# Performance work log

Measured on AMD Instinct MI355X. Metric: run time of the kernel, lower is better.

The kernel has to match this reference:

```python
import jax, jax.numpy as jnp
import numpy as np

N_NODES = 100000
N_EDGES = 1600000
MSG = 16
HID = 16
N_ETYPE = 8
N_CLASSES = 40


def setup_inputs() -> dict:
    key = jax.random.key(0)
    ks = jax.random.split(key, 11)
    return {
        "features": jax.random.normal(ks[0], (N_NODES, HID), dtype=jnp.float32),
        "src": jax.random.randint(ks[1], (N_EDGES,), 0, N_NODES),
        "dst": jax.random.randint(ks[2], (N_EDGES,), 0, N_NODES),
        "etype": jax.random.randint(ks[3], (N_EDGES,), 0, N_ETYPE),
        "edge_matrix": jax.random.normal(ks[4], (N_ETYPE, MSG * HID), dtype=jnp.float32) * 0.1,
        "w_ih": jax.random.normal(ks[5], (3 * HID, MSG), dtype=jnp.float32) * 0.1,
        "w_hh": jax.random.normal(ks[6], (3 * HID, HID), dtype=jnp.float32) * 0.1,
        "b_ih": jax.random.normal(ks[7], (3 * HID,), dtype=jnp.float32) * 0.1,
        "b_hh": jax.random.normal(ks[8], (3 * HID,), dtype=jnp.float32) * 0.1,
        "out_w": jax.random.normal(ks[9], (N_CLASSES, HID), dtype=jnp.float32) * 0.1,
        "out_b": jax.random.normal(ks[10], (N_CLASSES,), dtype=jnp.float32) * 0.1,
    }


def reference(features, src, dst, etype, edge_matrix, w_ih, w_hh, b_ih, b_hh, out_w, out_b):
    n = features.shape[0]
    # message: per-edge [MSG,HID] matrix (gathered by edge type) times src h
    A = edge_matrix[etype].reshape(-1, MSG, HID)          # [E, MSG, HID]
    msg = jnp.einsum('emh,eh->em', A, features[src])      # [E, MSG]
    # reduce: scatter-sum messages onto destination nodes
    m = jax.ops.segment_sum(msg, dst, num_segments=n)     # [N, MSG]
    # apply: one GRU step per node (PyTorch nn.GRU gate math)
    gi = m @ w_ih.T + b_ih                                # [N, 3*HID]
    gh = features @ w_hh.T + b_hh                         # [N, 3*HID]
    i_r, i_z, i_n = jnp.split(gi, 3, axis=-1)
    h_r, h_z, h_n = jnp.split(gh, 3, axis=-1)
    r = jax.nn.sigmoid(i_r + h_r)
    z = jax.nn.sigmoid(i_z + h_z)
    c = jnp.tanh(i_n + r * h_n)
    h = (1.0 - z) * c + z * features                      # [N, HID]
    return h @ out_w.T + out_b                            # [N, N_CLASSES]
```

## Files before the change

### kernel.cpp

```cpp
#include <hip/hip_runtime.h>
#include <math.h>

constexpr int N_NODES   = 100000;
constexpr int N_EDGES   = 1600000;
constexpr int MSG       = 16;
constexpr int HID       = 16;
constexpr int N_ETYPE   = 8;
constexpr int N_CLASSES = 40;

constexpr int CBSIZE   = 256;
constexpr int NBUCKET  = (N_NODES + CBSIZE - 1) / CBSIZE;
constexpr int SBSIZE   = 32;
constexpr int NSUB     = 8;
constexpr int NSB      = NBUCKET * NSUB;
constexpr int EPB      = 4096;
constexpr int NEBLK    = (N_EDGES + EPB - 1) / EPB;
constexpr int REC_CAP  = 5120;
constexpr int FGRID    = 1536;
constexpr int NSLOT    = 2048;
constexpr int A_STRIDE = 260;
constexpr int SRECC    = 1536;

typedef float vfloat4 __attribute__((ext_vector_type(4)));

__device__ __forceinline__ float sigmoidf_(float x) { return 1.0f / (1.0f + __expf(-x)); }
__device__ __forceinline__ float tanhf_(float x) { float e = __expf(2.0f * x); return 1.0f - 2.0f / (e + 1.0f); }

__device__ __forceinline__ unsigned f2bf(float f) {
    unsigned u = __float_as_uint(f);
    return (u + 0x7FFFu + ((u >> 16) & 1u)) >> 16;
}
__device__ __forceinline__ float bflo(unsigned u) { return __uint_as_float(u << 16); }
__device__ __forceinline__ float bfhi(unsigned u) { return __uint_as_float(u & 0xFFFF0000u); }

__global__ void __launch_bounds__(256) cvt_kernel(const float* __restrict__ features,
                                                  uint4* __restrict__ featb,
                                                  int* __restrict__ gcursor) {
    int i = blockIdx.x * 256 + threadIdx.x;
    if (i < NBUCKET) gcursor[i] = i * REC_CAP;
    else if (i == NBUCKET) gcursor[i] = FGRID;
    if (i * 8 >= N_NODES * HID) return;
    const float4* fp = reinterpret_cast<const float4*>(features + i * 8);
    float4 a = fp[0], b = fp[1];
    uint4 o;
    o.x = f2bf(a.x) | (f2bf(a.y) << 16);
    o.y = f2bf(a.z) | (f2bf(a.w) << 16);
    o.z = f2bf(b.x) | (f2bf(b.y) << 16);
    o.w = f2bf(b.z) | (f2bf(b.w) << 16);
    featb[i] = o;
}

__global__ void __launch_bounds__(512) partition_kernel(
    const int* __restrict__ src,
    const int* __restrict__ dst,
    const int* __restrict__ etype,
    int* __restrict__ gcursor,
    int* __restrict__ records)
{
    __shared__ int srec[EPB];
    __shared__ unsigned short sbkt[EPB];
    __shared__ int lh[NBUCKET];
    __shared__ int lscan[NBUCKET];
    __shared__ int gbarr[NBUCKET];
    __shared__ int wsum[8];

    int t = threadIdx.x;
    int base = blockIdx.x * EPB;

    for (int i = t; i < NBUCKET; i += 512) lh[i] = 0;
    __syncthreads();

    int rr[8]; int bb[8]; int rk[8];
    #pragma unroll
    for (int q = 0; q < 8; ++q) {
        int e = base + t + 512 * q;
        if (e < N_EDGES) {
            int d = dst[e];
            bb[q] = d >> 8;
            rr[q] = (src[e] << 11) | (etype[e] << 8) | (d & 255);
            rk[q] = atomicAdd(&lh[bb[q]], 1);
        } else bb[q] = -1;
    }
    __syncthreads();

    int i0 = t * 4;
    int v0 = 0, v1 = 0, v2 = 0, v3 = 0;
    if (i0     < NBUCKET) v0 = lh[i0];
    if (i0 + 1 < NBUCKET) v1 = lh[i0 + 1];
    if (i0 + 2 < NBUCKET) v2 = lh[i0 + 2];
    if (i0 + 3 < NBUCKET) v3 = lh[i0 + 3];
    int tsum = v0 + v1 + v2 + v3;

    int lane = t & 63, w = t >> 6;
    int inc = tsum;
    #pragma unroll
    for (int off = 1; off < 64; off <<= 1) {
        int u = __shfl_up(inc, off, 64);
        if (lane >= off) inc += u;
    }
    if (lane == 63) wsum[w] = inc;
    __syncthreads();
    int basew = 0;
    #pragma unroll
    for (int i = 0; i < 8; ++i) if (i < w) basew += wsum[i];
    int excl = basew + inc - tsum;

    if (i0     < NBUCKET) { lscan[i0]     = excl; gbarr[i0]     = v0 ? atomicAdd(&gcursor[i0],     v0) : 0; } excl += v0;
    if (i0 + 1 < NBUCKET) { lscan[i0 + 1] = excl; gbarr[i0 + 1] = v1 ? atomicAdd(&gcursor[i0 + 1], v1) : 0; } excl += v1;
    if (i0 + 2 < NBUCKET) { lscan[i0 + 2] = excl; gbarr[i0 + 2] = v2 ? atomicAdd(&gcursor[i0 + 2], v2) : 0; } excl += v2;
    if (i0 + 3 < NBUCKET) { lscan[i0 + 3] = excl; gbarr[i0 + 3] = v3 ? atomicAdd(&gcursor[i0 + 3], v3) : 0; }
    __syncthreads();

    #pragma unroll
    for (int q = 0; q < 8; ++q) {
        if (bb[q] >= 0) {
            int sidx = lscan[bb[q]] + rk[q];
            srec[sidx] = rr[q];
            sbkt[sidx] = (unsigned short)bb[q];
        }
    }
    __syncthreads();

    int cnt = min(EPB, N_EDGES - base);
    for (int s2 = t; s2 < cnt; s2 += 512) {
        int b2 = sbkt[s2];
        int pos = gbarr[b2] + (s2 - lscan[b2]);
        if (pos < (b2 + 1) * REC_CAP)
            records[pos] = srec[s2];
    }
}

__global__ void __launch_bounds__(256) partition2_kernel(
    const int* __restrict__ gcursor,
    const int* __restrict__ records,
    int* __restrict__ records2,
    int* __restrict__ slot_off)
{
    __shared__ int hist[NSLOT];
    __shared__ int wsum[4];
    __shared__ int srec[REC_CAP];

    int cb = blockIdx.x;
    int beg = cb * REC_CAP;
    int cnt = min(gcursor[cb] - beg, REC_CAP);
    int t = threadIdx.x;

    #pragma unroll
    for (int j = 0; j < 8; ++j) hist[t * 8 + j] = 0;
    __syncthreads();

    for (int i = t; i < cnt; i += 256) {
        int r = records[beg + i];
        atomicAdd(&hist[((r & 255) << 3) | ((r >> 8) & 7)], 1);
    }
    __syncthreads();

    int loc[8]; int tsum = 0;
    #pragma unroll
    for (int j = 0; j < 8; ++j) { loc[j] = hist[t * 8 + j]; tsum += loc[j]; }

    int lane = t & 63, w = t >> 6;
    int inc = tsum;
    #pragma unroll
    for (int off = 1; off < 64; off <<= 1) {
        int u = __shfl_up(inc, off, 64);
        if (lane >= off) inc += u;
    }
    if (lane == 63) wsum[w] = inc;
    __syncthreads();
    int basew = 0;
    #pragma unroll
    for (int i = 0; i < 4; ++i) if (i < w) basew += wsum[i];
    int excl = basew + inc - tsum;

    #pragma unroll
    for (int j = 0; j < 8; ++j) {
        slot_off[cb * (NSLOT + 1) + t * 8 + j] = beg + excl;
        hist[t * 8 + j] = excl;
        excl += loc[j];
    }
    if (t == 0) slot_off[cb * (NSLOT + 1) + NSLOT] = beg + cnt;
    __syncthreads();

    for (int i = t; i < cnt; i += 256) {
        int r = records[beg + i];
        int pos = atomicAdd(&hist[((r & 255) << 3) | ((r >> 8) & 7)], 1);
        srec[pos] = r;
    }
    __syncthreads();
    for (int i = t; i < cnt; i += 256) records2[beg + i] = srec[i];
}

__global__ void __launch_bounds__(256, 6) fused_kernel(
    const uint4* __restrict__ featb,
    const float* __restrict__ features,
    const int*   __restrict__ slot_off,
    const int*   __restrict__ records2,
    int*         __restrict__ wcnt,
    const float* __restrict__ edge_matrix,
    const float* __restrict__ w_ih,
    const float* __restrict__ w_hh,
    const float* __restrict__ b_ih,
    const float* __restrict__ b_hh,
    const float* __restrict__ out_w,
    const float* __restrict__ out_b,
    float*       __restrict__ out)
{
    __shared__ float A[N_ETYPE * A_STRIDE];
    __shared__ float wihL[3 * HID * 17];
    __shared__ float whhL[3 * HID * 17];
    __shared__ float outwL[N_CLASSES * 17];
    __shared__ float bihL[3 * HID];
    __shared__ float bhhL[3 * HID];
    __shared__ float outbL[N_CLASSES];
    __shared__ float hnT[HID][SBSIZE + 1];
    __shared__ int   uni[SRECC];
    __shared__ int   bS;

    int* srecL = uni;
    float* outS = reinterpret_cast<float*>(uni);

    int t = threadIdx.x;
    int dl = t >> 3, q = t & 7;
    const float4* feat4 = reinterpret_cast<const float4*>(features);

    if (t == 0) bS = blockIdx.x;

    for (int i = t; i < N_ETYPE * MSG * HID; i += 256)
        A[(i >> 8) * A_STRIDE + (i & 255)] = edge_matrix[i];
    for (int i = t; i < 3 * HID * MSG; i += 256) wihL[(i >> 4) * 17 + (i & 15)] = w_ih[i];
    for (int i = t; i < 3 * HID * HID; i += 256) whhL[(i >> 4) * 17 + (i & 15)] = w_hh[i];
    for (int i = t; i < N_CLASSES * HID; i += 256) outwL[(i >> 4) * 17 + (i & 15)] = out_w[i];
    if (t < 48) bihL[t] = b_ih[t];
    else if (t < 96) bhhL[t - 48] = b_hh[t - 48];
    else if (t < 136) outbL[t - 96] = out_b[t - 96];
    __syncthreads();

    for (;;) {
        int b = bS;
        if (b >= NSB) break;
        int nodeBase = b * SBSIZE;
        bool active = nodeBase < N_NODES;
        int cb = b >> 3, sb = b & 7;

        int S0 = 0, begin = 0, end = 0;
        if (active) {
            int sobase = cb * (NSLOT + 1) + sb * 256;
            S0 = slot_off[sobase];
            int S1 = slot_off[sobase + 256];
            begin = slot_off[sobase + t];
            end   = slot_off[sobase + t + 1];
            int lim = min(S1 - S0, SRECC);
            for (int i = t; i < lim; i += 256)
                srecL[i] = __builtin_nontemporal_load(records2 + S0 + i);
        }
        __syncthreads();

        if (t == 0) bS = atomicAdd(wcnt, 1);

        if (active) {
            float acc[16];
            #pragma unroll
            for (int k = 0; k < 16; ++k) acc[k] = 0.0f;
            for (int i = begin; i < end; ++i) {
                int li = i - S0;
                int rec = (li < SRECC) ? srecL[li] : records2[i];
                int sn = rec >> 11;
                uint4 ua = featb[2 * sn], ub = featb[2 * sn + 1];
                acc[0]  += bflo(ua.x); acc[1]  += bfhi(ua.x);
                acc[2]  += bflo(ua.y); acc[3]  += bfhi(ua.y);
                acc[4]  += bflo(ua.z); acc[5]  += bfhi(ua.z);
                acc[6]  += bflo(ua.w); acc[7]  += bfhi(ua.w);
                acc[8]  += bflo(ub.x); acc[9]  += bfhi(ub.x);
                acc[10] += bflo(ub.y); acc[11] += bfhi(ub.y);
                acc[12] += bflo(ub.z); acc[13] += bfhi(ub.z);
                acc[14] += bflo(ub.w); acc[15] += bfhi(ub.w);
            }

            float p[16];
            {
                const float* Aq = &A[q * A_STRIDE];
                #pragma unroll
                for (int mm = 0; mm < 16; ++mm) {
                    const float4* Ar = reinterpret_cast<const float4*>(Aq + mm * 16);
                    float4 x0 = Ar[0], x1 = Ar[1], x2 = Ar[2], x3 = Ar[3];
                    p[mm] = x0.x*acc[0]  + x0.y*acc[1]  + x0.z*acc[2]  + x0.w*acc[3]
                          + x1.x*acc[4]  + x1.y*acc[5]  + x1.z*acc[6]  + x1.w*acc[7]
                          + x2.x*acc[8]  + x2.y*acc[9]  + x2.z*acc[10] + x2.w*acc[11]
                          + x3.x*acc[12] + x3.y*acc[13] + x3.z*acc[14] + x3.w*acc[15];
                }
            }
            #pragma unroll
            for (int mm = 0; mm < 16; ++mm) {
                p[mm] += __shfl_xor(p[mm], 1, 64);
                p[mm] += __shfl_xor(p[mm], 2, 64);
                p[mm] += __shfl_xor(p[mm], 4, 64);
            }

            int n = nodeBase + dl;
            float hva[16];
            {
                const float4* hp = feat4 + (size_t)n * 4;
                float4 h0 = hp[0], h1 = hp[1], h2 = hp[2], h3 = hp[3];
                hva[0]=h0.x; hva[1]=h0.y; hva[2]=h0.z; hva[3]=h0.w;
                hva[4]=h1.x; hva[5]=h1.y; hva[6]=h1.z; hva[7]=h1.w;
                hva[8]=h2.x; hva[9]=h2.y; hva[10]=h2.z; hva[11]=h2.w;
                hva[12]=h3.x; hva[13]=h3.y; hva[14]=h3.z; hva[15]=h3.w;
            }
            #pragma unroll
            for (int jj = 0; jj < 2; ++jj) {
                int j = 2 * q + jj;
                float ir  = bihL[j];
                float iz  = bihL[j + HID];
                float inn = bihL[j + 2 * HID];
                float hr  = bhhL[j];
                float hz  = bhhL[j + HID];
                float hnn = bhhL[j + 2 * HID];
                const float* wir = &wihL[j * 17];
                const float* wiz = &wihL[(j + HID) * 17];
                const float* win = &wihL[(j + 2 * HID) * 17];
                const float* whr = &whhL[j * 17];
                const float* whz = &whhL[(j + HID) * 17];
                const float* whn = &whhL[(j + 2 * HID) * 17];
                #pragma unroll
                for (int k = 0; k < HID; ++k) {
                    ir  += wir[k] * p[k];
                    iz  += wiz[k] * p[k];
                    inn += win[k] * p[k];
                    hr  += whr[k] * hva[k];
                    hz  += whz[k] * hva[k];
                    hnn += whn[k] * hva[k];
                }
                float rg = sigmoidf_(ir + hr);
                float zg = sigmoidf_(iz + hz);
                float cg = tanhf_(inn + rg * hnn);
                float hj = features[(size_t)n * HID + j];
                hnT[j][dl] = (1.0f - zg) * cg + zg * hj;
            }
        }
        __syncthreads();

        if (active) {
            float hh[HID];
            #pragma unroll
            for (int k = 0; k < HID; ++k) hh[k] = hnT[k][dl];
            #pragma unroll
            for (int cc = 0; cc < 5; ++cc) {
                int c = 5 * q + cc;
                float a2 = outbL[c];
                const float* wr = &outwL[c * 17];
                #pragma unroll
                for (int k = 0; k < HID; ++k) a2 += wr[k] * hh[k];
                outS[dl * 44 + c] = a2;
            }
        }
        __syncthreads();

        if (active) {
            vfloat4* ob4 = reinterpret_cast<vfloat4*>(out + (size_t)nodeBase * N_CLASSES);
            #pragma unroll
            for (int rep = 0; rep < 2; ++rep) {
                int i = t + rep * 256;
                if (i < SBSIZE * N_CLASSES / 4) {
                    int node = i / 10, qq = i - node * 10;
                    vfloat4 v = *reinterpret_cast<const vfloat4*>(&outS[node * 44 + qq * 4]);
                    __builtin_nontemporal_store(v, ob4 + i);
                }
            }
        }
        __syncthreads();
    }
}

extern "C" void kernel_launch(void* const* d_in, const int* in_sizes, int n_in,
                              void* d_out, int out_size, void* d_ws, size_t ws_size,
                              hipStream_t stream) {
    const float* features    = (const float*)d_in[0];
    const int*   src         = (const int*)  d_in[1];
    const int*   dst         = (const int*)  d_in[2];
    const int*   etype       = (const int*)  d_in[3];
    const float* edge_matrix = (const float*)d_in[4];
    const float* w_ih        = (const float*)d_in[5];
    const float* w_hh        = (const float*)d_in[6];
    const float* b_ih        = (const float*)d_in[7];
    const float* b_hh        = (const float*)d_in[8];
    const float* out_w       = (const float*)d_in[9];
    const float* out_b       = (const float*)d_in[10];
    float* out = (float*)d_out;

    int* gcursor  = (int*)d_ws;
    int* wcnt     = gcursor + NBUCKET;
    int* slot_off = wcnt + 1;
    int* records  = slot_off + NBUCKET * (NSLOT + 1);
    int* records2 = records + NBUCKET * REC_CAP;
    size_t featb_off = ((size_t)((char*)(records2 + NBUCKET * REC_CAP) - (char*)d_ws) + 15) & ~15ull;
    uint4* featb = (uint4*)((char*)d_ws + featb_off);

    cvt_kernel<<<(N_NODES * HID / 8 + 255) / 256, 256, 0, stream>>>(features, featb, gcursor);
    partition_kernel<<<NEBLK, 512, 0, stream>>>(src, dst, etype, gcursor, records);
    partition2_kernel<<<NBUCKET, 256, 0, stream>>>(gcursor, records, records2, slot_off);
    fused_kernel<<<FGRID, 256, 0, stream>>>(
        featb, features, slot_off, records2, wcnt, edge_matrix,
        w_ih, w_hh, b_ih, b_hh, out_w, out_b, out);
}
```

Measured before the change: 121.0 us.

## Retune partition sizes, drop LDS record staging and nontemporal stores in fused kernel

Halves edges per partition block, doubles partition2 threads, lowers the fused persistent grid, removes the LDS staging of sorted records (reading records2 straight from global), moves the work-counter atomic later, and replaces nontemporal output stores with plain float4 stores. The intent is to cut LDS footprint and synchronisation in the fused kernel and raise parallelism in the partition stages. The cost is uncoalesced per-thread global record reads and more partition blocks issuing global atomics.

```diff
diff --git a/kernel.cpp b/kernel.cpp
--- a/kernel.cpp
+++ b/kernel.cpp
@@ -13,15 +13,13 @@
 constexpr int SBSIZE   = 32;
 constexpr int NSUB     = 8;
 constexpr int NSB      = NBUCKET * NSUB;
-constexpr int EPB      = 4096;
+constexpr int EPB      = 2048;
+constexpr int EPT      = EPB / 512;
 constexpr int NEBLK    = (N_EDGES + EPB - 1) / EPB;
 constexpr int REC_CAP  = 5120;
-constexpr int FGRID    = 1536;
+constexpr int FGRID    = 1043;
 constexpr int NSLOT    = 2048;
 constexpr int A_STRIDE = 260;
-constexpr int SRECC    = 1536;
-
-typedef float vfloat4 __attribute__((ext_vector_type(4)));
 
 __device__ __forceinline__ float sigmoidf_(float x) { return 1.0f / (1.0f + __expf(-x)); }
 __device__ __forceinline__ float tanhf_(float x) { float e = __expf(2.0f * x); return 1.0f - 2.0f / (e + 1.0f); }
@@ -70,9 +68,9 @@
     for (int i = t; i < NBUCKET; i += 512) lh[i] = 0;
     __syncthreads();
 
-    int rr[8]; int bb[8]; int rk[8];
-    #pragma unroll
-    for (int q = 0; q < 8; ++q) {
+    int rr[EPT]; int bb[EPT]; int rk[EPT];
+    #pragma unroll
+    for (int q = 0; q < EPT; ++q) {
         int e = base + t + 512 * q;
         if (e < N_EDGES) {
             int d = dst[e];
@@ -112,7 +110,7 @@
     __syncthreads();
 
     #pragma unroll
-    for (int q = 0; q < 8; ++q) {
+    for (int q = 0; q < EPT; ++q) {
         if (bb[q] >= 0) {
             int sidx = lscan[bb[q]] + rk[q];
             srec[sidx] = rr[q];
@@ -130,14 +128,14 @@
     }
 }
 
-__global__ void __launch_bounds__(256) partition2_kernel(
+__global__ void __launch_bounds__(512) partition2_kernel(
     const int* __restrict__ gcursor,
     const int* __restrict__ records,
     int* __restrict__ records2,
     int* __restrict__ slot_off)
 {
     __shared__ int hist[NSLOT];
-    __shared__ int wsum[4];
+    __shared__ int wsum[8];
     __shared__ int srec[REC_CAP];
 
     int cb = blockIdx.x;
@@ -146,18 +144,18 @@
     int t = threadIdx.x;
 
     #pragma unroll
-    for (int j = 0; j < 8; ++j) hist[t * 8 + j] = 0;
-    __syncthreads();
-
-    for (int i = t; i < cnt; i += 256) {
+    for (int j = 0; j < 4; ++j) hist[t * 4 + j] = 0;
+    __syncthreads();
+
+    for (int i = t; i < cnt; i += 512) {
         int r = records[beg + i];
         atomicAdd(&hist[((r & 255) << 3) | ((r >> 8) & 7)], 1);
     }
     __syncthreads();
 
-    int loc[8]; int tsum = 0;
-    #pragma unroll
-    for (int j = 0; j < 8; ++j) { loc[j] = hist[t * 8 + j]; tsum += loc[j]; }
+    int loc[4]; int tsum = 0;
+    #pragma unroll
+    for (int j = 0; j < 4; ++j) { loc[j] = hist[t * 4 + j]; tsum += loc[j]; }
 
     int lane = t & 63, w = t >> 6;
     int inc = tsum;
@@ -170,25 +168,25 @@
     __syncthreads();
     int basew = 0;
     #pragma unroll
-    for (int i = 0; i < 4; ++i) if (i < w) basew += wsum[i];
+    for (int i = 0; i < 8; ++i) if (i < w) basew += wsum[i];
     int excl = basew + inc - tsum;
 
     #pragma unroll
-    for (int j = 0; j < 8; ++j) {
-        slot_off[cb * (NSLOT + 1) + t * 8 + j] = beg + excl;
-        hist[t * 8 + j] = excl;
+    for (int j = 0; j < 4; ++j) {
+        slot_off[cb * (NSLOT + 1) + t * 4 + j] = beg + excl;
+        hist[t * 4 + j] = excl;
         excl += loc[j];
     }
     if (t == 0) slot_off[cb * (NSLOT + 1) + NSLOT] = beg + cnt;
     __syncthreads();
 
-    for (int i = t; i < cnt; i += 256) {
+    for (int i = t; i < cnt; i += 512) {
         int r = records[beg + i];
         int pos = atomicAdd(&hist[((r & 255) << 3) | ((r >> 8) & 7)], 1);
         srec[pos] = r;
     }
     __syncthreads();
-    for (int i = t; i < cnt; i += 256) records2[beg + i] = srec[i];
+    for (int i = t; i < cnt; i += 512) records2[beg + i] = srec[i];
 }
 
 __global__ void __launch_bounds__(256, 6) fused_kernel(
@@ -214,11 +212,8 @@
     __shared__ float bhhL[3 * HID];
     __shared__ float outbL[N_CLASSES];
     __shared__ float hnT[HID][SBSIZE + 1];
-    __shared__ int   uni[SRECC];
+    __shared__ float outS[SBSIZE * 44];
     __shared__ int   bS;
-
-    int* srecL = uni;
-    float* outS = reinterpret_cast<float*>(uni);
 
     int t = threadIdx.x;
     int dl = t >> 3, q = t & 7;
@@ -243,28 +238,15 @@
         bool active = nodeBase < N_NODES;
         int cb = b >> 3, sb = b & 7;
 
-        int S0 = 0, begin = 0, end = 0;
         if (active) {
-            int sobase = cb * (NSLOT + 1) + sb * 256;
-            S0 = slot_off[sobase];
-            int S1 = slot_off[sobase + 256];
-            begin = slot_off[sobase + t];
-            end   = slot_off[sobase + t + 1];
-            int lim = min(S1 - S0, SRECC);
-            for (int i = t; i < lim; i += 256)
-                srecL[i] = __builtin_nontemporal_load(records2 + S0 + i);
-        }
-        __syncthreads();
-
-        if (t == 0) bS = atomicAdd(wcnt, 1);
-
-        if (active) {
+            int go = cb * (NSLOT + 1) + sb * 256 + t;
+            int begin = slot_off[go], end = slot_off[go + 1];
+
             float acc[16];
             #pragma unroll
             for (int k = 0; k < 16; ++k) acc[k] = 0.0f;
             for (int i = begin; i < end; ++i) {
-                int li = i - S0;
-                int rec = (li < SRECC) ? srecL[li] : records2[i];
+                int rec = records2[i];
                 int sn = rec >> 11;
                 uint4 ua = featb[2 * sn], ub = featb[2 * sn + 1];
                 acc[0]  += bflo(ua.x); acc[1]  += bfhi(ua.x);
@@ -340,6 +322,8 @@
         }
         __syncthreads();
 
+        if (t == 0) bS = atomicAdd(wcnt, 1);
+
         if (active) {
             float hh[HID];
             #pragma unroll
@@ -357,14 +341,13 @@
         __syncthreads();
 
         if (active) {
-            vfloat4* ob4 = reinterpret_cast<vfloat4*>(out + (size_t)nodeBase * N_CLASSES);
+            float4* ob4 = reinterpret_cast<float4*>(out + (size_t)nodeBase * N_CLASSES);
             #pragma unroll
             for (int rep = 0; rep < 2; ++rep) {
                 int i = t + rep * 256;
                 if (i < SBSIZE * N_CLASSES / 4) {
                     int node = i / 10, qq = i - node * 10;
-                    vfloat4 v = *reinterpret_cast<const vfloat4*>(&outS[node * 44 + qq * 4]);
-                    __builtin_nontemporal_store(v, ob4 + i);
+                    ob4[i] = *reinterpret_cast<const float4*>(&outS[node * 44 + qq * 4]);
                 }
             }
         }
@@ -398,7 +381,7 @@
 
     cvt_kernel<<<(N_NODES * HID / 8 + 255) / 256, 256, 0, stream>>>(features, featb, gcursor);
     partition_kernel<<<NEBLK, 512, 0, stream>>>(src, dst, etype, gcursor, records);
-    partition2_kernel<<<NBUCKET, 256, 0, stream>>>(gcursor, records, records2, slot_off);
+    partition2_kernel<<<NBUCKET, 512, 0, stream>>>(gcursor, records, records2, slot_off);
     fused_kernel<<<FGRID, 256, 0, stream>>>(
         featb, features, slot_off, records2, wcnt, edge_matrix,
         w_ih, w_hh, b_ih, b_hh, out_w, out_b, out);
```

New measurement: 148.8 us. 1.23x slower.
